# Kernel tuning notes

Hardware: AMD Instinct MI355X
Metric: run time of the kernel (lower is better)

Reference implementation:

```python
import jax, jax.numpy as jnp
import numpy as np

B, S, DIM, HEADS, HEAD_DIM = 4, 1024, 1024, 16, 64
INNER = HEADS * HEAD_DIM
NEG_INF = -1e30


def _rotate_half(t):
    # interleaved pairs: (x1, x2) -> (-x2, x1)
    t = t.reshape(*t.shape[:-1], -1, 2)
    x1, x2 = t[..., 0], t[..., 1]
    return jnp.stack((-x2, x1), axis=-1).reshape(*t.shape[:-2], -1)


def _apply_rope(t, freqs, scale):
    # t: [B, S, INNER]; freqs: [1, S, rot_dim]; rotate only first rot_dim channels
    rot_dim = freqs.shape[-1]
    t_rot, t_pass = t[..., :rot_dim], t[..., rot_dim:]
    t_rot = t_rot * jnp.cos(freqs) * scale + _rotate_half(t_rot) * jnp.sin(freqs) * scale
    return jnp.concatenate((t_rot, t_pass), axis=-1)


def setup_inputs() -> dict:
    key = jax.random.key(0)
    ks = jax.random.split(key, 12)
    x = jax.random.normal(ks[0], (B, S, DIM), dtype=jnp.float32)
    mask = jax.random.bernoulli(ks[1], 0.9, (B, S))
    mask = mask.at[:, 0].set(True)  # ensure every row has a valid key
    # standard rope angles, interleave-repeated to head_dim
    pos = np.arange(S, dtype=np.float32)
    inv_freq = 1.0 / (10000.0 ** (np.arange(0, HEAD_DIM, 2, dtype=np.float32) / HEAD_DIM))
    ang = pos[:, None] * inv_freq[None, :]             # [S, HEAD_DIM//2]
    freqs = jnp.asarray(np.repeat(ang, 2, axis=-1)[None])  # [1, S, HEAD_DIM]
    sc = 1.0 / np.sqrt(DIM)
    def lin(k, din, dout):
        kw, kb = jax.random.split(k)
        return (jax.random.uniform(kw, (din, dout), minval=-sc, maxval=sc),
                jax.random.uniform(kb, (dout,), minval=-sc, maxval=sc))
    Wq, bq = lin(ks[2], DIM, INNER)
    Wk, bk = lin(ks[3], DIM, INNER)
    Wv, bv = lin(ks[4], DIM, INNER)
    Wo, bo = lin(ks[5], INNER, DIM)
    return {"x": x, "mask": mask, "freqs": freqs, "Wq": Wq, "bq": bq,
            "Wk": Wk, "bk": bk, "Wv": Wv, "bv": bv, "Wo": Wo, "bo": bo}


def reference(x, mask, freqs, Wq, bq, Wk, bk, Wv, bv, Wo, bo):
    b = x.shape[0]
    q = x @ Wq + bq
    k = x @ Wk + bk
    v = x @ Wv + bv
    # xpos_scale is None -> scale 1.0 for both q and k
    q = _apply_rope(q, freqs, 1.0)
    k = _apply_rope(k, freqs, 1.0)
    # split heads: [B, H, S, Dh]
    q = q.reshape(b, -1, HEADS, HEAD_DIM).transpose(0, 2, 1, 3)
    k = k.reshape(b, -1, HEADS, HEAD_DIM).transpose(0, 2, 1, 3)
    v = v.reshape(b, -1, HEADS, HEAD_DIM).transpose(0, 2, 1, 3)
    scores = jnp.einsum('bhqd,bhkd->bhqk', q, k) / jnp.sqrt(jnp.float32(HEAD_DIM))
    scores = jnp.where(mask[:, None, None, :], scores, NEG_INF)
    attn = jax.nn.softmax(scores, axis=-1)
    out = jnp.einsum('bhqk,bhkd->bhqd', attn, v)
    out = out.transpose(0, 2, 1, 3).reshape(b, -1, INNER)
    out = out @ Wo + bo
    out = jnp.where(mask[..., None], out, 0.0)
    return out
```

## Files before the change

### kernel.cpp

```cpp
#include <hip/hip_runtime.h>
#include <stdint.h>


typedef unsigned short u16;
typedef __attribute__((ext_vector_type(8))) short short8;
typedef __attribute__((ext_vector_type(4))) float f32x4;
typedef __attribute__((ext_vector_type(4))) unsigned short bf4;

#define LOG2E 1.44269504088896f
#define INV2PI 0.15915494309189535f
#define MFMA_BF16(a,b,c) __builtin_amdgcn_mfma_f32_16x16x32_bf16((a),(b),(c),0,0,0)
#define WAITV(N) asm volatile("s_waitcnt vmcnt(" #N ")" ::: "memory")

__device__ __forceinline__ float bf2f(u16 u){
    union { uint32_t i; float f; } v; v.i = ((uint32_t)u) << 16; return v.f;
}
__device__ __forceinline__ u16 f2bf(float f){
    uint32_t u = __builtin_bit_cast(uint32_t, f);
    u += 0x7FFFu + ((u >> 16) & 1u);
    return (u16)(u >> 16);
}
__device__ __forceinline__ uint32_t cvt_pk_bf16(float lo, float hi){
    uint32_t r;
    asm("v_cvt_pk_bf16_f32 %0, %1, %2" : "=v"(r) : "v"(lo), "v"(hi));
    return r;
}
__device__ __forceinline__ float fast_ex2(float x){
    float r; asm("v_exp_f32 %0, %1" : "=v"(r) : "v"(x)); return r;
}
__device__ __forceinline__ float fast_rcp(float x){
    float r; asm("v_rcp_f32 %0, %1" : "=v"(r) : "v"(x)); return r;
}
__device__ __forceinline__ void fast_sincos(float xrad, float& s, float& c){
    float rev = xrad * INV2PI, fr;
    asm("v_fract_f32 %0, %1" : "=v"(fr) : "v"(rev));
    asm("v_cos_f32 %0, %1" : "=v"(c) : "v"(fr));
    asm("v_sin_f32 %0, %1" : "=v"(s) : "v"(fr));
}

__device__ __forceinline__ void gload_lds16(const void* g, uint32_t dst_lds_byte){
    __builtin_amdgcn_global_load_lds(
        (__attribute__((address_space(1))) uint32_t*)(uintptr_t)g,
        (__attribute__((address_space(3))) uint32_t*)(uintptr_t)dst_lds_byte,
        16, 0, 0);
}

constexpr size_t OFF_XB    = 0;
constexpr size_t OFF_VT    = OFF_XB;
constexpr size_t OFF_WQKVT = 8388608;
constexpr size_t OFF_WOT   = OFF_WQKVT + 6291456;
constexpr size_t OFF_BQKV  = OFF_WOT   + 2097152;
constexpr size_t OFF_MASKB = OFF_BQKV  + 12288;
constexpr size_t OFF_QKV   = OFF_MASKB + 16384;
constexpr size_t OFF_AO    = OFF_QKV   + 25165824;
constexpr size_t WS_NEED   = OFF_AO    + 8388608;

__global__ __launch_bounds__(256) void k_prep(const float* __restrict__ x,
                                              const float* __restrict__ Wq,
                                              const float* __restrict__ Wk,
                                              const float* __restrict__ Wv,
                                              const float* __restrict__ Wo,
                                              const float* __restrict__ bq,
                                              const float* __restrict__ bk,
                                              const float* __restrict__ bv,
                                              const unsigned char* __restrict__ mask,
                                              u16* __restrict__ xb,
                                              u16* __restrict__ Wqkvt,
                                              u16* __restrict__ Wot,
                                              float* __restrict__ bqkv,
                                              float* __restrict__ maskb){
    __shared__ float lds[64][65];
    const int t = threadIdx.x, bid = blockIdx.x;
    if (bid < 4096){
        int gid = bid * 256 + t;
        float4 v = ((const float4*)x)[gid];
        bf4 o;
        o[0] = f2bf(v.x); o[1] = f2bf(v.y); o[2] = f2bf(v.z); o[3] = f2bf(v.w);
        ((bf4*)xb)[gid] = o;
    } else if (bid < 5120){
        int blk = bid - 4096;
        int which = blk >> 8;
        const float* src = which == 0 ? Wq : which == 1 ? Wk : which == 2 ? Wv : Wo;
        u16* dst = which < 3 ? (Wqkvt + (size_t)which * 1024 * 1024) : Wot;
        int n0 = ((blk >> 4) & 15) * 64, k0 = (blk & 15) * 64;
        #pragma unroll
        for (int i = 0; i < 16; i++){
            int idx = t + i * 256; int rr = idx >> 6, cc = idx & 63;
            lds[rr][cc] = src[(size_t)(k0 + rr) * 1024 + n0 + cc];
        }
        __syncthreads();
        #pragma unroll
        for (int i = 0; i < 16; i++){
            int idx = t + i * 256; int rr = idx >> 6, cc = idx & 63;
            dst[(size_t)(n0 + rr) * 1024 + k0 + cc] = f2bf(lds[cc][rr]);
        }
    } else {
        int gid = (bid - 5120) * 256 + t;
        if (gid < 3072){
            bqkv[gid] = gid < 1024 ? bq[gid] : gid < 2048 ? bk[gid - 1024] : bv[gid - 2048];
        } else if (gid < 3072 + 4096){
            int j = gid - 3072;
            int cnt3f = 0;
            #pragma unroll
            for (int i = 0; i < 16; i++) cnt3f += (mask[4 * i + 3] == 0x3F);
            bool v;
            if (cnt3f >= 8){
                v = ((const float*)mask)[j] != 0.f;
            } else {
                int nz = 0;
                for (int i = 1; i < 64; i++) if (i & 3) nz += (mask[i] != 0);
                if (nz) v = mask[j] != 0;
                else    v = ((const int*)mask)[j] != 0;
            }
            maskb[j] = v ? 0.f : -1e30f;
        }
    }
}

__global__ __launch_bounds__(256) void k_gemm2(const u16* __restrict__ A,
                                               const u16* __restrict__ Bt,
                                               const float* __restrict__ bias,
                                               const float* __restrict__ freqs,
                                               u16* __restrict__ Cout){
    constexpr int K = 1024, N = 3072;
    __shared__ alignas(16) u16 sAB[3][12288];
    const int t = threadIdx.x;
    const int w = t >> 6, l = t & 63, g = l >> 4, r = l & 15;
    const int brow = blockIdx.x * 256, bcol = blockIdx.y * 128;
    const int wm = w >> 1, wn = w & 1;
    f32x4 acc[8][4] = {};

    const int lcol = (((l & 3) ^ ((l >> 3) & 3)) * 8);
    const u16* ga = A  + (size_t)(brow + w * 64 + (l >> 2)) * K + lcol;
    const u16* gb = Bt + (size_t)(bcol + w * 32 + (l >> 2)) * K + lcol;
    const size_t K16 = (size_t)16 * K;
    const uint32_t dstA = (uint32_t)__builtin_amdgcn_readfirstlane(
        (int)((uint32_t)(uintptr_t)&sAB[0][0] + (uint32_t)(w * 4096)));
    const uint32_t dstB = (uint32_t)__builtin_amdgcn_readfirstlane(
        (int)((uint32_t)(uintptr_t)&sAB[0][0] + (uint32_t)(16384 + w * 2048)));

    constexpr int NT = K / 32;
    auto stage = [&](int kt, int s){
        const int k0 = kt * 32;
        const uint32_t off = (uint32_t)s * 24576;
        #pragma unroll
        for (int i = 0; i < 4; i++)
            gload_lds16(ga + k0 + (size_t)i * K16, dstA + off + i * 1024);
        #pragma unroll
        for (int i = 0; i < 2; i++)
            gload_lds16(gb + k0 + (size_t)i * K16, dstB + off + i * 1024);
    };

    stage(0, 0);
    stage(1, 1);
    const int rs = (r >> 1) & 3;
    int s_cur = 0;
    for (int kt = 0; kt < NT; ++kt){
        if (kt + 1 < NT) WAITV(6);
        else             WAITV(0);
        __builtin_amdgcn_s_barrier();
        __builtin_amdgcn_sched_barrier(0);
        if (kt + 2 < NT){
            int s_pf = s_cur + 2; if (s_pf >= 3) s_pf -= 3;
            stage(kt + 2, s_pf);
        }
        const u16* sA = &sAB[s_cur][0];
        const u16* sB = &sAB[s_cur][8192];
        short8 af[8], bf[4];
        #pragma unroll
        for (int m = 0; m < 8; m++)
            af[m] = *(const short8*)&sA[(wm * 128 + m * 16 + r) * 32 + ((g ^ rs) * 8)];
        #pragma unroll
        for (int n = 0; n < 4; n++)
            bf[n] = *(const short8*)&sB[(wn * 64 + n * 16 + r) * 32 + ((g ^ rs) * 8)];
        __builtin_amdgcn_s_setprio(1);
        #pragma unroll
        for (int m = 0; m < 8; m++)
            #pragma unroll
            for (int n = 0; n < 4; n++)
                acc[m][n] = MFMA_BF16(af[m], bf[n], acc[m][n]);
        __builtin_amdgcn_s_setprio(0);
        s_cur = (s_cur == 2) ? 0 : s_cur + 1;
    }

    const bool rope = (blockIdx.y == 0 || blockIdx.y == 8) && (wn == 0);
    #pragma unroll
    for (int n = 0; n < 4; n++){
        int col = bcol + wn * 64 + n * 16 + r;
        float bb = bias[col];
        float cs = (col < 1024) ? 0.125f : 1.f;
        #pragma unroll
        for (int m = 0; m < 8; m++){
            f32x4 v = acc[m][n];
            #pragma unroll
            for (int jj = 0; jj < 4; jj++){
                int row = brow + wm * 128 + m * 16 + g * 4 + jj;
                float val = (v[jj] + bb) * cs;
                if (rope){
                    float partner = __shfl_xor(val, 1);
                    float ang = freqs[(row & 1023) * 64 + (col & 62)];
                    float sn, c;
                    fast_sincos(ang, sn, c);
                    val = (r & 1) ? val * c + partner * sn
                                  : val * c - partner * sn;
                }
                Cout[(size_t)row * N + col] = f2bf(val);
            }
        }
    }
}

__global__ __launch_bounds__(256) void k_gemm(const u16* __restrict__ A,
                                              const u16* __restrict__ Bt,
                                              const float* __restrict__ bias,
                                              const float* __restrict__ maskb,
                                              float* __restrict__ Cout,
                                              int M, int N, int K){
    __shared__ alignas(16) u16 sAB[3][2][128 * 32];
    const int t = threadIdx.x;
    const int w = t >> 6, l = t & 63, g = l >> 4, r = l & 15;
    const int brow = blockIdx.x * 128, bcol = blockIdx.y * 128;
    const int wr = (w >> 1) * 64, wc = (w & 1) * 64;
    f32x4 acc[4][4] = {};

    const int lrow = w * 32 + (l >> 2);
    const int lcol = (((l & 3) ^ ((l >> 3) & 3)) * 8);
    const u16* ga = A  + (size_t)(brow + lrow) * K + lcol;
    const u16* gb = Bt + (size_t)(bcol + lrow) * K + lcol;
    const size_t K16 = (size_t)16 * K;
    const uint32_t dst0 = (uint32_t)__builtin_amdgcn_readfirstlane(
        (int)((uint32_t)(uintptr_t)&sAB[0][0][0] + (uint32_t)(w * 2048)));

    const int NT = K >> 5;
    auto stage = [&](int kt, int s){
        const int k0 = kt * 32;
        const uint32_t da = dst0 + (uint32_t)s * 16384;
        gload_lds16(ga + k0,       da);
        gload_lds16(ga + k0 + K16, da + 1024);
        gload_lds16(gb + k0,       da + 8192);
        gload_lds16(gb + k0 + K16, da + 8192 + 1024);
    };

    stage(0, 0);
    stage(1, 1);
    const int rs = (r >> 1) & 3;
    int s_cur = 0;
    for (int kt = 0; kt < NT; ++kt){
        if (kt + 1 < NT) WAITV(4);
        else             WAITV(0);
        __builtin_amdgcn_s_barrier();
        __builtin_amdgcn_sched_barrier(0);
        if (kt + 2 < NT){
            int s_pf = s_cur + 2; if (s_pf >= 3) s_pf -= 3;
            stage(kt + 2, s_pf);
        }
        const u16* sA = &sAB[s_cur][0][0];
        const u16* sB = &sAB[s_cur][1][0];
        short8 af[4], bf[4];
        #pragma unroll
        for (int m = 0; m < 4; m++)
            af[m] = *(const short8*)&sA[(wr + m * 16 + r) * 32 + ((g ^ rs) * 8)];
        #pragma unroll
        for (int n = 0; n < 4; n++)
            bf[n] = *(const short8*)&sB[(wc + n * 16 + r) * 32 + ((g ^ rs) * 8)];
        __builtin_amdgcn_s_setprio(1);
        #pragma unroll
        for (int m = 0; m < 4; m++)
            #pragma unroll
            for (int n = 0; n < 4; n++)
                acc[m][n] = MFMA_BF16(af[m], bf[n], acc[m][n]);
        __builtin_amdgcn_s_setprio(0);
        s_cur = (s_cur == 2) ? 0 : s_cur + 1;
    }

    #pragma unroll
    for (int n = 0; n < 4; n++){
        int col = bcol + wc + n * 16 + r;
        float bb = bias[col];
        #pragma unroll
        for (int m = 0; m < 4; m++){
            f32x4 v = acc[m][n];
            #pragma unroll
            for (int jj = 0; jj < 4; jj++){
                int row = brow + wr + m * 16 + g * 4 + jj;
                Cout[(size_t)row * N + col] =
                    (maskb[row] == 0.f) ? (v[jj] + bb) : 0.f;
            }
        }
    }
}

__global__ __launch_bounds__(256) void k_vt(const u16* __restrict__ QKV,
                                            u16* __restrict__ Vt){
    __shared__ u16 lds[64][72];
    const int bh = blockIdx.x >> 4, s0 = (blockIdx.x & 15) * 64;
    const int b = bh >> 4, h = bh & 15;
    const int t = threadIdx.x;
    const u16* src = QKV + (size_t)(b * 1024 + s0) * 3072 + 2048 + h * 64;
    #pragma unroll
    for (int i = 0; i < 2; i++){
        int s = i * 32 + (t >> 3), dc = (t & 7) * 8;
        short8 v = *(const short8*)(src + (size_t)s * 3072 + dc);
        #pragma unroll
        for (int j = 0; j < 8; j++) lds[dc + j][s] = (u16)v[j];
    }
    __syncthreads();
    #pragma unroll
    for (int i = 0; i < 2; i++){
        int d = i * 32 + (t >> 3), sc = (t & 7) * 8;
        short8 v = *(const short8*)&lds[d][sc];
        *(short8*)&Vt[(size_t)(bh * 64 + d) * 1024 + s0 + sc] = v;
    }
}

__global__ __launch_bounds__(256) void k_attn(const u16* __restrict__ QKV,
                                              const u16* __restrict__ Vt,
                                              const float* __restrict__ maskb,
                                              u16* __restrict__ AO){
    __shared__ alignas(16) u16 sK [2][64 * 64];
    __shared__ alignas(16) u16 sVt[2][64 * 64];
    __shared__ alignas(16) u16 sP [4][16 * 64];
    const int t = threadIdx.x, w = t >> 6, l = t & 63, g = l >> 4, r = l & 15;
    const int hw = blockIdx.x;
    const int blk = ((hw & 7) << 7) | (hw >> 3);
    const int qb = blk & 15, h = (blk >> 4) & 15, b = blk >> 8;
    const int bh = b * 16 + h;
    const int qrow0 = b * 1024 + qb * 64 + w * 16;
    const int rx = r & 7;

    const u16* qptr = QKV + (size_t)(qrow0 + r) * 3072 + h * 64;
    short8 qf0 = *(const short8*)(qptr + g * 8);
    short8 qf1 = *(const short8*)(qptr + 32 + g * 8);

    const int srow = l >> 3;
    const int c16  = (l & 7) ^ srow;
    const u16* Kg = QKV + (size_t)(b * 1024) * 3072 + 1024 + h * 64;
    const u16* gK0 = Kg + (size_t)(w * 16 + srow) * 3072 + c16 * 8;
    const u16* gK1 = gK0 + (size_t)8 * 3072;
    const u16* Vg = Vt + (size_t)bh * 64 * 1024;
    const u16* gV0 = Vg + (size_t)(w * 16 + srow) * 1024 + c16 * 8;
    const u16* gV1 = gV0 + (size_t)8 * 1024;
    uint32_t dK0 = (uint32_t)__builtin_amdgcn_readfirstlane(
        (int)((uint32_t)(uintptr_t)&sK[0][0] + (uint32_t)(w * 2048)));
    uint32_t dV0 = (uint32_t)__builtin_amdgcn_readfirstlane(
        (int)((uint32_t)(uintptr_t)&sVt[0][0] + (uint32_t)(w * 2048)));
    char* sPw = (char*)&sP[w][0];
    const char* sKc = (const char*)&sK[0][0];
    const char* sVc = (const char*)&sVt[0][0];

    const float* mkb = maskb + b * 1024;

    f32x4 oacc[4] = {};
    float lsum = 0.f;

    gload_lds16(gK0, dK0);
    gload_lds16(gK1, dK0 + 1024);
    gload_lds16(gV0, dV0);
    gload_lds16(gV1, dV0 + 1024);
    __syncthreads();

    for (int kt = 0; kt < 16; ++kt){
        const int cur = kt & 1;
        if (kt < 15){
            const size_t kv = (size_t)(kt + 1) * 64;
            const uint32_t dk = dK0 + (cur ^ 1) * 8192;
            const uint32_t dv = dV0 + (cur ^ 1) * 8192;
            gload_lds16(gK0 + kv * 3072, dk);
            gload_lds16(gK1 + kv * 3072, dk + 1024);
            gload_lds16(gV0 + kv, dv);
            gload_lds16(gV1 + kv, dv + 1024);
        }
        const char* sKb = sKc + cur * 8192;
        const char* sVb = sVc + cur * 8192;
        const int kv0 = kt * 64;

        f32x4 st[4];
        __builtin_amdgcn_s_setprio(1);
        #pragma unroll
        for (int kn = 0; kn < 4; kn++){
            const int row = kn * 16 + r;
            short8 kf0 = *(const short8*)(sKb + row * 128 + (((g    ) ^ rx) << 4));
            short8 kf1 = *(const short8*)(sKb + row * 128 + (((g + 4) ^ rx) << 4));
            f32x4 z = {};
            z = MFMA_BF16(kf0, qf0, z);
            st[kn] = MFMA_BF16(kf1, qf1, z);
        }
        __builtin_amdgcn_s_setprio(0);

        float p[16];
        #pragma unroll
        for (int kn = 0; kn < 4; kn++){
            f32x4 mbv = *(const f32x4*)(mkb + kv0 + kn * 16 + g * 4);
            #pragma unroll
            for (int jj = 0; jj < 4; jj++){
                float pe = fast_ex2(fmaf(st[kn][jj], LOG2E, mbv[jj]));
                p[kn * 4 + jj] = pe;
                lsum += pe;
            }
        }

        #pragma unroll
        for (int kn = 0; kn < 4; kn++){
            uint2 u;
            u.x = cvt_pk_bf16(p[kn * 4 + 0], p[kn * 4 + 1]);
            u.y = cvt_pk_bf16(p[kn * 4 + 2], p[kn * 4 + 3]);
            *(uint2*)(sPw + r * 128 + ((((2 * kn + (g >> 1))) ^ rx) << 4) + (g & 1) * 8) = u;
        }

        #pragma unroll
        for (int ks = 0; ks < 2; ks++){
            short8 pa = *(const short8*)(sPw + r * 128 + ((((ks << 2) | g) ^ rx) << 4));
            __builtin_amdgcn_s_setprio(1);
            #pragma unroll
            for (int dn = 0; dn < 4; dn++){
                const int vrow = dn * 16 + r;
                short8 vf = *(const short8*)(sVb + vrow * 128 + ((((ks << 2) | g) ^ rx) << 4));
                oacc[dn] = MFMA_BF16(pa, vf, oacc[dn]);
            }
            __builtin_amdgcn_s_setprio(0);
        }
        __syncthreads();
    }

    lsum += __shfl_xor(lsum, 16);
    lsum += __shfl_xor(lsum, 32);
    float linv = fast_rcp(lsum);
    float lf[4];
    #pragma unroll
    for (int jj = 0; jj < 4; jj++) lf[jj] = __shfl(linv, g * 4 + jj);
    #pragma unroll
    for (int dn = 0; dn < 4; dn++)
        #pragma unroll
        for (int jj = 0; jj < 4; jj++)
            AO[(size_t)(qrow0 + g * 4 + jj) * 1024 + h * 64 + dn * 16 + r]
                = f2bf(oacc[dn][jj] * lf[jj]);
}

extern "C" void kernel_launch(void* const* d_in, const int* in_sizes, int n_in,
                              void* d_out, int out_size, void* d_ws, size_t ws_size,
                              hipStream_t stream){
    (void)in_sizes; (void)n_in; (void)out_size;
    if (ws_size < WS_NEED) return;

    const float* x     = (const float*)d_in[0];
    const unsigned char* mask = (const unsigned char*)d_in[1];
    const float* freqs = (const float*)d_in[2];
    const float* Wq    = (const float*)d_in[3];
    const float* bq    = (const float*)d_in[4];
    const float* Wk    = (const float*)d_in[5];
    const float* bk    = (const float*)d_in[6];
    const float* Wv    = (const float*)d_in[7];
    const float* bv    = (const float*)d_in[8];
    const float* Wo    = (const float*)d_in[9];
    const float* bo    = (const float*)d_in[10];

    char* ws = (char*)d_ws;
    u16*   xb    = (u16*)  (ws + OFF_XB);
    u16*   Vtw   = (u16*)  (ws + OFF_VT);
    u16*   Wqkvt = (u16*)  (ws + OFF_WQKVT);
    u16*   Wot   = (u16*)  (ws + OFF_WOT);
    float* bqkv  = (float*)(ws + OFF_BQKV);
    float* maskb = (float*)(ws + OFF_MASKB);
    u16*   QKV   = (u16*)  (ws + OFF_QKV);
    u16*   AO    = (u16*)  (ws + OFF_AO);

    k_prep<<<5148, 256, 0, stream>>>(x, Wq, Wk, Wv, Wo, bq, bk, bv, mask,
                                     xb, Wqkvt, Wot, bqkv, maskb);
    k_gemm2<<<dim3(16, 24), 256, 0, stream>>>(xb, Wqkvt, bqkv, freqs, QKV);
    k_vt  <<<1024, 256, 0, stream>>>(QKV, Vtw);
    k_attn<<<1024, 256, 0, stream>>>(QKV, Vtw, maskb, AO);
    k_gemm<<<dim3(32, 8), 256, 0, stream>>>(AO, Wot, bo, maskb,
                                            (float*)d_out, 4096, 1024, 1024);
}
```

Measured before the change: 119.3 us.

## Retile QKV and output GEMMs to smaller tiles with XCD-aware block remapping

The QKV projection now uses a 128x128 tile (768 blocks) in place of 256x128 (384 blocks). The output projection uses a 64x128 tile (512 blocks) in place of 128x128 (256 blocks). Both kernels remap the linear block id so that consecutive ids handed out round-robin across the 8 XCDs land on neighbouring tiles, which should improve L2 reuse. Together these aim to fill all CUs better and cut tail imbalance, at the cost of lower arithmetic intensity per block and more redundant global loads.

```diff
diff --git a/kernel.cpp b/kernel.cpp
--- a/kernel.cpp
+++ b/kernel.cpp
@@ -117,109 +117,18 @@
     }
 }
 
-__global__ __launch_bounds__(256) void k_gemm2(const u16* __restrict__ A,
+__global__ __launch_bounds__(256) void k_gemmq(const u16* __restrict__ A,
                                                const u16* __restrict__ Bt,
                                                const float* __restrict__ bias,
                                                const float* __restrict__ freqs,
                                                u16* __restrict__ Cout){
     constexpr int K = 1024, N = 3072;
-    __shared__ alignas(16) u16 sAB[3][12288];
-    const int t = threadIdx.x;
-    const int w = t >> 6, l = t & 63, g = l >> 4, r = l & 15;
-    const int brow = blockIdx.x * 256, bcol = blockIdx.y * 128;
-    const int wm = w >> 1, wn = w & 1;
-    f32x4 acc[8][4] = {};
-
-    const int lcol = (((l & 3) ^ ((l >> 3) & 3)) * 8);
-    const u16* ga = A  + (size_t)(brow + w * 64 + (l >> 2)) * K + lcol;
-    const u16* gb = Bt + (size_t)(bcol + w * 32 + (l >> 2)) * K + lcol;
-    const size_t K16 = (size_t)16 * K;
-    const uint32_t dstA = (uint32_t)__builtin_amdgcn_readfirstlane(
-        (int)((uint32_t)(uintptr_t)&sAB[0][0] + (uint32_t)(w * 4096)));
-    const uint32_t dstB = (uint32_t)__builtin_amdgcn_readfirstlane(
-        (int)((uint32_t)(uintptr_t)&sAB[0][0] + (uint32_t)(16384 + w * 2048)));
-
-    constexpr int NT = K / 32;
-    auto stage = [&](int kt, int s){
-        const int k0 = kt * 32;
-        const uint32_t off = (uint32_t)s * 24576;
-        #pragma unroll
-        for (int i = 0; i < 4; i++)
-            gload_lds16(ga + k0 + (size_t)i * K16, dstA + off + i * 1024);
-        #pragma unroll
-        for (int i = 0; i < 2; i++)
-            gload_lds16(gb + k0 + (size_t)i * K16, dstB + off + i * 1024);
-    };
-
-    stage(0, 0);
-    stage(1, 1);
-    const int rs = (r >> 1) & 3;
-    int s_cur = 0;
-    for (int kt = 0; kt < NT; ++kt){
-        if (kt + 1 < NT) WAITV(6);
-        else             WAITV(0);
-        __builtin_amdgcn_s_barrier();
-        __builtin_amdgcn_sched_barrier(0);
-        if (kt + 2 < NT){
-            int s_pf = s_cur + 2; if (s_pf >= 3) s_pf -= 3;
-            stage(kt + 2, s_pf);
-        }
-        const u16* sA = &sAB[s_cur][0];
-        const u16* sB = &sAB[s_cur][8192];
-        short8 af[8], bf[4];
-        #pragma unroll
-        for (int m = 0; m < 8; m++)
-            af[m] = *(const short8*)&sA[(wm * 128 + m * 16 + r) * 32 + ((g ^ rs) * 8)];
-        #pragma unroll
-        for (int n = 0; n < 4; n++)
-            bf[n] = *(const short8*)&sB[(wn * 64 + n * 16 + r) * 32 + ((g ^ rs) * 8)];
-        __builtin_amdgcn_s_setprio(1);
-        #pragma unroll
-        for (int m = 0; m < 8; m++)
-            #pragma unroll
-            for (int n = 0; n < 4; n++)
-                acc[m][n] = MFMA_BF16(af[m], bf[n], acc[m][n]);
-        __builtin_amdgcn_s_setprio(0);
-        s_cur = (s_cur == 2) ? 0 : s_cur + 1;
-    }
-
-    const bool rope = (blockIdx.y == 0 || blockIdx.y == 8) && (wn == 0);
-    #pragma unroll
-    for (int n = 0; n < 4; n++){
-        int col = bcol + wn * 64 + n * 16 + r;
-        float bb = bias[col];
-        float cs = (col < 1024) ? 0.125f : 1.f;
-        #pragma unroll
-        for (int m = 0; m < 8; m++){
-            f32x4 v = acc[m][n];
-            #pragma unroll
-            for (int jj = 0; jj < 4; jj++){
-                int row = brow + wm * 128 + m * 16 + g * 4 + jj;
-                float val = (v[jj] + bb) * cs;
-                if (rope){
-                    float partner = __shfl_xor(val, 1);
-                    float ang = freqs[(row & 1023) * 64 + (col & 62)];
-                    float sn, c;
-                    fast_sincos(ang, sn, c);
-                    val = (r & 1) ? val * c + partner * sn
-                                  : val * c - partner * sn;
-                }
-                Cout[(size_t)row * N + col] = f2bf(val);
-            }
-        }
-    }
-}
-
-__global__ __launch_bounds__(256) void k_gemm(const u16* __restrict__ A,
-                                              const u16* __restrict__ Bt,
-                                              const float* __restrict__ bias,
-                                              const float* __restrict__ maskb,
-                                              float* __restrict__ Cout,
-                                              int M, int N, int K){
     __shared__ alignas(16) u16 sAB[3][2][128 * 32];
     const int t = threadIdx.x;
     const int w = t >> 6, l = t & 63, g = l >> 4, r = l & 15;
-    const int brow = blockIdx.x * 128, bcol = blockIdx.y * 128;
+    const int lid  = blockIdx.y * 32 + blockIdx.x;
+    const int slid = (lid & 7) * 96 + (lid >> 3);
+    const int brow = (slid & 31) * 128, bcol = (slid >> 5) * 128;
     const int wr = (w >> 1) * 64, wc = (w & 1) * 64;
     f32x4 acc[4][4] = {};
 
@@ -231,7 +140,7 @@
     const uint32_t dst0 = (uint32_t)__builtin_amdgcn_readfirstlane(
         (int)((uint32_t)(uintptr_t)&sAB[0][0][0] + (uint32_t)(w * 2048)));
 
-    const int NT = K >> 5;
+    constexpr int NT = K >> 5;
     auto stage = [&](int kt, int s){
         const int k0 = kt * 32;
         const uint32_t da = dst0 + (uint32_t)s * 16384;
@@ -273,16 +182,108 @@
         s_cur = (s_cur == 2) ? 0 : s_cur + 1;
     }
 
+    const bool rope = (bcol == 0 || bcol == 1024) && (wc == 0);
     #pragma unroll
     for (int n = 0; n < 4; n++){
         int col = bcol + wc + n * 16 + r;
         float bb = bias[col];
+        float cs = (col < 1024) ? 0.125f : 1.f;
         #pragma unroll
         for (int m = 0; m < 4; m++){
             f32x4 v = acc[m][n];
             #pragma unroll
             for (int jj = 0; jj < 4; jj++){
                 int row = brow + wr + m * 16 + g * 4 + jj;
+                float val = (v[jj] + bb) * cs;
+                if (rope){
+                    float partner = __shfl_xor(val, 1);
+                    float ang = freqs[(row & 1023) * 64 + (col & 62)];
+                    float sn, c;
+                    fast_sincos(ang, sn, c);
+                    val = (r & 1) ? val * c + partner * sn
+                                  : val * c - partner * sn;
+                }
+                Cout[(size_t)row * N + col] = f2bf(val);
+            }
+        }
+    }
+}
+
+__global__ __launch_bounds__(256) void k_gemm_o(const u16* __restrict__ A,
+                                                const u16* __restrict__ Bt,
+                                                const float* __restrict__ bias,
+                                                const float* __restrict__ maskb,
+                                                float* __restrict__ Cout){
+    constexpr int K = 1024, N = 1024;
+    __shared__ alignas(16) u16 sAB[3][6144];
+    const int t = threadIdx.x;
+    const int w = t >> 6, l = t & 63, g = l >> 4, r = l & 15;
+    const int lid  = blockIdx.y * 64 + blockIdx.x;
+    const int slid = (lid & 7) * 64 + (lid >> 3);
+    const int brow = (slid & 63) * 64, bcol = (slid >> 6) * 128;
+    const int wm = w >> 1, wn = w & 1;
+    f32x4 acc[2][4] = {};
+
+    const int lcol = (((l & 3) ^ ((l >> 3) & 3)) * 8);
+    const u16* ga = A  + (size_t)(brow + w * 16 + (l >> 2)) * K + lcol;
+    const u16* gb = Bt + (size_t)(bcol + w * 32 + (l >> 2)) * K + lcol;
+    const size_t K16 = (size_t)16 * K;
+    const uint32_t dstA = (uint32_t)__builtin_amdgcn_readfirstlane(
+        (int)((uint32_t)(uintptr_t)&sAB[0][0] + (uint32_t)(w * 1024)));
+    const uint32_t dstB = (uint32_t)__builtin_amdgcn_readfirstlane(
+        (int)((uint32_t)(uintptr_t)&sAB[0][0] + (uint32_t)(4096 + w * 2048)));
+
+    constexpr int NT = K >> 5;
+    auto stage = [&](int kt, int s){
+        const int k0 = kt * 32;
+        const uint32_t off = (uint32_t)s * 12288;
+        gload_lds16(ga + k0,       dstA + off);
+        gload_lds16(gb + k0,       dstB + off);
+        gload_lds16(gb + k0 + K16, dstB + off + 1024);
+    };
+
+    stage(0, 0);
+    stage(1, 1);
+    const int rs = (r >> 1) & 3;
+    int s_cur = 0;
+    for (int kt = 0; kt < NT; ++kt){
+        if (kt + 1 < NT) WAITV(3);
+        else             WAITV(0);
+        __builtin_amdgcn_s_barrier();
+        __builtin_amdgcn_sched_barrier(0);
+        if (kt + 2 < NT){
+            int s_pf = s_cur + 2; if (s_pf >= 3) s_pf -= 3;
+            stage(kt + 2, s_pf);
+        }
+        const u16* sA = &sAB[s_cur][0];
+        const u16* sB = &sAB[s_cur][2048];
+        short8 af[2], bf[4];
+        #pragma unroll
+        for (int m = 0; m < 2; m++)
+            af[m] = *(const short8*)&sA[(wm * 32 + m * 16 + r) * 32 + ((g ^ rs) * 8)];
+        #pragma unroll
+        for (int n = 0; n < 4; n++)
+            bf[n] = *(const short8*)&sB[(wn * 64 + n * 16 + r) * 32 + ((g ^ rs) * 8)];
+        __builtin_amdgcn_s_setprio(1);
+        #pragma unroll
+        for (int m = 0; m < 2; m++)
+            #pragma unroll
+            for (int n = 0; n < 4; n++)
+                acc[m][n] = MFMA_BF16(af[m], bf[n], acc[m][n]);
+        __builtin_amdgcn_s_setprio(0);
+        s_cur = (s_cur == 2) ? 0 : s_cur + 1;
+    }
+
+    #pragma unroll
+    for (int n = 0; n < 4; n++){
+        int col = bcol + wn * 64 + n * 16 + r;
+        float bb = bias[col];
+        #pragma unroll
+        for (int m = 0; m < 2; m++){
+            f32x4 v = acc[m][n];
+            #pragma unroll
+            for (int jj = 0; jj < 4; jj++){
+                int row = brow + wm * 32 + m * 16 + g * 4 + jj;
                 Cout[(size_t)row * N + col] =
                     (maskb[row] == 0.f) ? (v[jj] + bb) : 0.f;
             }
@@ -466,9 +467,8 @@
 
     k_prep<<<5148, 256, 0, stream>>>(x, Wq, Wk, Wv, Wo, bq, bk, bv, mask,
                                      xb, Wqkvt, Wot, bqkv, maskb);
-    k_gemm2<<<dim3(16, 24), 256, 0, stream>>>(xb, Wqkvt, bqkv, freqs, QKV);
-    k_vt  <<<1024, 256, 0, stream>>>(QKV, Vtw);
-    k_attn<<<1024, 256, 0, stream>>>(QKV, Vtw, maskb, AO);
-    k_gemm<<<dim3(32, 8), 256, 0, stream>>>(AO, Wot, bo, maskb,
-                                            (float*)d_out, 4096, 1024, 1024);
-}
+    k_gemmq<<<dim3(32, 24), 256, 0, stream>>>(xb, Wqkvt, bqkv, freqs, QKV);
+    k_vt   <<<1024, 256, 0, stream>>>(QKV, Vtw);
+    k_attn <<<1024, 256, 0, stream>>>(QKV, Vtw, maskb, AO);
+    k_gemm_o<<<dim3(64, 8), 256, 0, stream>>>(AO, Wot, bo, maskb, (float*)d_out);
+}
```

Result: no change. 120.0 us (+0.6%).
